# Kernel optimization log

Hardware: AMD Instinct MI355X
Metric: run time of the kernel (lower is better)

Reference implementation:

```python
import jax, jax.numpy as jnp
import numpy as np
import math

M = 0.5
S = 64.0
COS_M = math.cos(M)
SIN_M = math.sin(M)
THRESHOLD = math.cos(math.pi - M)
MM = math.sin(math.pi - M) * M

B, D, N_CLASSES = 512, 512, 100000


def setup_inputs() -> dict:
    key = jax.random.key(0)
    k1, k2, k3 = jax.random.split(key, 3)
    embeddings = jax.random.normal(k1, (B, D), dtype=jnp.float32)
    labels = jax.random.randint(k2, (B,), 0, N_CLASSES, dtype=jnp.int32)
    kernel = jax.random.normal(k3, (D, N_CLASSES), dtype=jnp.float32) * 0.05
    t = jnp.zeros((), dtype=jnp.float32)
    return {"embeddings": embeddings, "labels": labels, "kernel": kernel, "t": t}


def reference(embeddings, labels, kernel, t):
    # L2 normalize embeddings (rows) and kernel (columns)
    emb = embeddings / jnp.linalg.norm(embeddings, axis=1, keepdims=True)
    kn = kernel / jnp.linalg.norm(kernel, axis=0, keepdims=True)
    cos_theta = jnp.clip(emb @ kn, -1.0, 1.0)  # [B, C]

    b = cos_theta.shape[0]
    rows = jnp.arange(b)
    target_logit = cos_theta[rows, labels][:, None]  # [B, 1]
    sin_theta = jnp.sqrt(1.0 - jnp.square(target_logit))
    cos_theta_m = target_logit * COS_M - sin_theta * SIN_M  # [B, 1]

    mask = cos_theta > cos_theta_m  # [B, C] hard examples
    final_target_logit = jnp.where(target_logit > THRESHOLD,
                                   cos_theta_m, target_logit - MM)  # [B, 1]

    # EMA update of t (assigned before the hard-example scaling in TF code)
    new_t = 0.01 * jnp.mean(target_logit) + 0.99 * t

    # hard examples: c -> c * (t + c); others unchanged
    cos_theta = jnp.where(mask, cos_theta * (new_t + cos_theta), cos_theta)
    # overwrite label column with the margin-adjusted target logit
    cos_theta = cos_theta.at[rows, labels].set(final_target_logit[:, 0])
    return cos_theta * S
```

## Files before the change

### kernel.cpp

```cpp
#include <hip/hip_runtime.h>
#include <hip/hip_bf16.h>
#include <cstdint>
#include <cstddef>

#define C_N 100000
#define B_N 512
#define D_N 512

#define COS_M_F   0.87758256189037276f
#define SIN_M_F   0.47942553860420301f
#define THRESH_F  (-0.87758256189037276f)
#define MM_F      0.23971276930210150f
#define S_F       64.0f

typedef __attribute__((ext_vector_type(8))) short short8;
typedef __attribute__((ext_vector_type(4))) float f32x4;

__device__ __forceinline__ unsigned short f2bf(float f) {
  unsigned u = __float_as_uint(f);
  u = u + 0x7fffu + ((u >> 16) & 1u);
  return (unsigned short)(u >> 16);
}

__device__ __forceinline__ float wave_sum(float v) {
#pragma unroll
  for (int o = 32; o > 0; o >>= 1) v += __shfl_down(v, o, 64);
  return v;
}

__device__ __forceinline__ void lds_load16(const void* g, void* l) {
  __builtin_amdgcn_global_load_lds(
      (const __attribute__((address_space(1))) unsigned int*)g,
      (__attribute__((address_space(3))) unsigned int*)l, 16, 0, 0);
}

__launch_bounds__(512)
__global__ void knorm2_k(const float* __restrict__ Kp, float* __restrict__ cninv,
                         unsigned short* __restrict__ Knt) {
  __shared__ __align__(16) unsigned short Tl[64 * 512];
  __shared__ float ssum[32][64];
  __shared__ float cns[64];

  const int t = threadIdx.x;
  const int j0 = blockIdx.x * 64;
  const int jq = t & 15;
  const int dr = t >> 4;
  const int jcol = min((j0 >> 2) + jq, (C_N >> 2) - 1);
  const float4* __restrict__ Kv = (const float4*)Kp;

  float4 v[16];
#pragma unroll
  for (int i = 0; i < 16; ++i)
    v[i] = Kv[(size_t)(dr * 16 + i) * (C_N / 4) + jcol];

  float s0 = 0.f, s1 = 0.f, s2 = 0.f, s3 = 0.f;
#pragma unroll
  for (int i = 0; i < 16; ++i) {
    s0 = fmaf(v[i].x, v[i].x, s0);
    s1 = fmaf(v[i].y, v[i].y, s1);
    s2 = fmaf(v[i].z, v[i].z, s2);
    s3 = fmaf(v[i].w, v[i].w, s3);
  }
  ssum[dr][jq * 4 + 0] = s0;
  ssum[dr][jq * 4 + 1] = s1;
  ssum[dr][jq * 4 + 2] = s2;
  ssum[dr][jq * 4 + 3] = s3;
  __syncthreads();
  if (t < 64) {
    float s = 0.f;
#pragma unroll
    for (int d = 0; d < 32; ++d) s += ssum[d][t];
    float r = rsqrtf(fmaxf(s, 1e-30f));
    cns[t] = r;
    if (j0 + t < C_N) cninv[j0 + t] = r;
  }
  __syncthreads();

  const float r0 = cns[jq * 4 + 0];
  const float r1 = cns[jq * 4 + 1];
  const float r2 = cns[jq * 4 + 2];
  const float r3 = cns[jq * 4 + 3];
#pragma unroll
  for (int g = 0; g < 4; ++g) {
    const int ch = dr * 2 + (g >> 1);
    const int sub = (g & 1) * 8;
#pragma unroll
    for (int c = 0; c < 4; ++c) {
      const int j = jq * 4 + c;
      const float rc = (c == 0) ? r0 : (c == 1) ? r1 : (c == 2) ? r2 : r3;
      unsigned lo, hi;
      lo = (unsigned)f2bf(v[g * 4 + 0][c] * rc) | ((unsigned)f2bf(v[g * 4 + 1][c] * rc) << 16);
      hi = (unsigned)f2bf(v[g * 4 + 2][c] * rc) | ((unsigned)f2bf(v[g * 4 + 3][c] * rc) << 16);
      const int phys = ch ^ (j & 7);
      *(uint2*)((char*)Tl + j * 1024 + phys * 16 + sub) = make_uint2(lo, hi);
    }
  }
  __syncthreads();

  const int jr = t >> 3;
  const int dc = t & 7;
  const int jg = j0 + jr;
  if (jg < C_N) {
#pragma unroll
    for (int s = 0; s < 8; ++s) {
      const int phys = (s * 8) + (dc ^ (jr & 7));
      uint4 val = *(const uint4*)((const char*)Tl + jr * 1024 + phys * 16);
      *(uint4*)(&Knt[(size_t)jg * D_N + s * 64 + dc * 8]) = val;
    }
  }
}

__global__ void embnorm_k(const float* __restrict__ emb, unsigned short* __restrict__ embn,
                          float* __restrict__ rinv) {
  int row = blockIdx.x;
  int t = threadIdx.x;
  float4 v = ((const float4*)(emb + (size_t)row * D_N))[t];
  float ss = v.x * v.x + v.y * v.y + v.z * v.z + v.w * v.w;
  ss = wave_sum(ss);
  __shared__ float red[2];
  if ((t & 63) == 0) red[t >> 6] = ss;
  __syncthreads();
  float tot = red[0] + red[1];
  float ri = rsqrtf(tot);
  if (t == 0) rinv[row] = ri;
  ushort4 o;
  o.x = f2bf(v.x * ri); o.y = f2bf(v.y * ri); o.z = f2bf(v.z * ri); o.w = f2bf(v.w * ri);
  ((ushort4*)(embn + (size_t)row * D_N))[t] = o;
}

__global__ void target2_k(const float* __restrict__ emb, const float* __restrict__ Kp,
                          const float* __restrict__ rinv, const int* __restrict__ labels,
                          float* __restrict__ target, float* __restrict__ ctm,
                          float* __restrict__ ft) {
  int row = blockIdx.x;
  int t = threadIdx.x;
  int lab = labels[row];
  float p = 0.f, ss = 0.f;
  for (int d = t; d < D_N; d += 256) {
    float kv = Kp[(size_t)d * C_N + lab];
    p = fmaf(emb[(size_t)row * D_N + d], kv, p);
    ss = fmaf(kv, kv, ss);
  }
  p = wave_sum(p);
  ss = wave_sum(ss);
  __shared__ float redp[4], reds[4];
  if ((t & 63) == 0) { redp[t >> 6] = p; reds[t >> 6] = ss; }
  __syncthreads();
  if (t == 0) {
    float dot = redp[0] + redp[1] + redp[2] + redp[3];
    float sums = reds[0] + reds[1] + reds[2] + reds[3];
    float tg = dot * rinv[row] * rsqrtf(fmaxf(sums, 1e-30f));
    tg = fminf(fmaxf(tg, -1.f), 1.f);
    float st = sqrtf(fmaxf(1.f - tg * tg, 0.f));
    float cm = tg * COS_M_F - st * SIN_M_F;
    float f = (tg > THRESH_F) ? cm : (tg - MM_F);
    target[row] = tg;
    ctm[row] = cm;
    ft[row] = f;
  }
}

__global__ void newt_k(const float* __restrict__ target, const float* __restrict__ t_in,
                       float* __restrict__ newt) {
  int t = threadIdx.x;
  float v = target[t];
  v = wave_sum(v);
  __shared__ float red[8];
  if ((t & 63) == 0) red[t >> 6] = v;
  __syncthreads();
  if (t == 0) {
    float s = 0.f;
#pragma unroll
    for (int i = 0; i < 8; ++i) s += red[i];
    *newt = 0.01f * (s / (float)B_N) + 0.99f * t_in[0];
  }
}

__launch_bounds__(256, 4)
__global__ void gemm10_k(const unsigned short* __restrict__ Knt,
                         const unsigned short* __restrict__ embn,
                         const int* __restrict__ labels,
                         const float* __restrict__ ctm, const float* __restrict__ ft,
                         const float* __restrict__ newt_p, float* __restrict__ out) {
  __shared__ __align__(16) unsigned short Al[2][8192];
  __shared__ __align__(16) unsigned short Bb[2][2048];

  const int t = threadIdx.x;
  const int l = t & 63, w = t >> 6;
  const int mi = blockIdx.x & 1;
  const int jb = blockIdx.x >> 1;
  const int m0 = mi * 256;
  const int j0 = jb * 64;

  const int sidx = (l & 7) ^ (l >> 3);
  const int r0 = ((l >> 3) << 1) | (sidx >> 2);
  const int kc8 = (sidx & 3) * 8;

  const unsigned short* asrc = embn + (size_t)(m0 + w * 64 + r0) * D_N + kc8;
  const unsigned short* bsrc = Knt + (size_t)(j0 + w * 16 + r0) * D_N + kc8;

#pragma unroll
  for (int p = 0; p < 4; ++p)
    lds_load16(asrc + p * 16 * D_N, &Al[0][w * 2048 + p * 512]);
  lds_load16(bsrc, &Bb[0][w * 512]);
  __syncthreads();

  const int wr = w >> 1, wc = w & 1;
  const int lq = l >> 4, lr = l & 15;
  const int s16 = ((((lr & 1) << 2) | lq) ^ (lr >> 1)) << 4;
  const int rh = lr >> 1;

  f32x4 acc[8][2];
#pragma unroll
  for (int mb = 0; mb < 8; ++mb) {
    acc[mb][0] = 0;
    acc[mb][1] = 0;
  }

#pragma unroll
  for (int it = 0; it < 16; ++it) {
    const int cur = it & 1, nxt = cur ^ 1;
    if (it < 15) {
      const int k0 = (it + 1) * 32;
#pragma unroll
      for (int p = 0; p < 4; ++p)
        lds_load16(asrc + p * 16 * D_N + k0, &Al[nxt][w * 2048 + p * 512]);
      lds_load16(bsrc + k0, &Bb[nxt][w * 512]);
    }
    const char* Ab = (const char*)Al[cur];
    const char* Bt = (const char*)Bb[cur];
    short8 b0 = *(const short8*)(Bt + ((wc * 16 + 0 + rh) << 7) + s16);
    short8 b1 = *(const short8*)(Bt + ((wc * 16 + 8 + rh) << 7) + s16);
#pragma unroll
    for (int mb = 0; mb < 8; ++mb) {
      short8 a = *(const short8*)(Ab + ((wr * 64 + mb * 8 + rh) << 7) + s16);
      acc[mb][0] = __builtin_amdgcn_mfma_f32_16x16x32_bf16(a, b0, acc[mb][0], 0, 0, 0);
      acc[mb][1] = __builtin_amdgcn_mfma_f32_16x16x32_bf16(a, b1, acc[mb][1], 0, 0, 0);
    }
    __syncthreads();
  }

  const float newt = *newt_p;
  const int jn0 = j0 + wc * 32 + lr;
  const int jn1 = jn0 + 16;
#pragma unroll
  for (int mb = 0; mb < 8; ++mb) {
    const int ibase = wr * 128 + mb * 16 + 4 * lq;
#pragma unroll
    for (int r = 0; r < 4; ++r) {
      const int grow = m0 + ibase + r;
      const int lab = labels[grow];
      const float cm = ctm[grow];
      const float f = ft[grow];
      {
        float c = fminf(fmaxf(acc[mb][0][r], -1.f), 1.f);
        float o = (c > cm) ? c * (newt + c) : c;
        o = (jn0 == lab) ? f : o;
        if (jn0 < C_N) out[(size_t)grow * C_N + jn0] = o * S_F;
      }
      {
        float c = fminf(fmaxf(acc[mb][1][r], -1.f), 1.f);
        float o = (c > cm) ? c * (newt + c) : c;
        o = (jn1 == lab) ? f : o;
        if (jn1 < C_N) out[(size_t)grow * C_N + jn1] = o * S_F;
      }
    }
  }
}

extern "C" void kernel_launch(void* const* d_in, const int* in_sizes, int n_in,
                              void* d_out, int out_size, void* d_ws, size_t ws_size,
                              hipStream_t stream) {
  (void)in_sizes; (void)n_in; (void)out_size; (void)ws_size;
  const float* emb = (const float*)d_in[0];
  const int* labels = (const int*)d_in[1];
  const float* Kp = (const float*)d_in[2];
  const float* t_in = (const float*)d_in[3];
  float* out = (float*)d_out;

  char* wsp = (char*)d_ws;
  const size_t KNT_BYTES = (size_t)100096 * D_N * 2;
  unsigned short* Knt = (unsigned short*)(wsp + 0);
  unsigned short* embn = (unsigned short*)(wsp + KNT_BYTES);
  float* cninv  = (float*)(wsp + KNT_BYTES + 524288);
  float* target = (float*)(wsp + KNT_BYTES + 524288 + 400000);
  float* ctm    = (float*)(wsp + KNT_BYTES + 524288 + 400000 + 2048);
  float* ft     = (float*)(wsp + KNT_BYTES + 524288 + 400000 + 2 * 2048);
  float* rinv   = (float*)(wsp + KNT_BYTES + 524288 + 400000 + 3 * 2048);
  float* newt   = (float*)(wsp + KNT_BYTES + 524288 + 400000 + 4 * 2048);

  knorm2_k<<<(C_N + 63) / 64, 512, 0, stream>>>(Kp, cninv, Knt);
  embnorm_k<<<B_N, 128, 0, stream>>>(emb, embn, rinv);
  target2_k<<<B_N, 256, 0, stream>>>(emb, Kp, rinv, labels, target, ctm, ft);
  newt_k<<<1, 512, 0, stream>>>(target, t_in, newt);
  const int jblocks = (C_N + 63) / 64;
  gemm10_k<<<jblocks * 2, 256, 0, stream>>>(Knt, embn, labels, ctm, ft, newt, out);
}
```

Measured before the change: 194.2 us.

## Deepen GEMM load pipeline to triple-buffered A and quad-buffered B stages

Replaces the double-buffered LDS pipeline in the fused GEMM/epilogue kernel with a 3-stage A buffer and 4-stage B buffer. Loads are issued two or three iterations ahead, and synchronisation is managed by hand with explicit vmcnt waits and raw barriers instead of __syncthreads. The goal is to hide global-to-LDS latency better. In exchange it uses more LDS, and the launch bound drops from 4 to 2 blocks per CU, which may reduce occupancy. The hand-counted waits are fragile.

```diff
diff --git a/kernel.cpp b/kernel.cpp
--- a/kernel.cpp
+++ b/kernel.cpp
@@ -176,14 +176,14 @@
   }
 }
 
-__launch_bounds__(256, 4)
-__global__ void gemm10_k(const unsigned short* __restrict__ Knt,
+__launch_bounds__(256, 2)
+__global__ void gemm11_k(const unsigned short* __restrict__ Knt,
                          const unsigned short* __restrict__ embn,
                          const int* __restrict__ labels,
                          const float* __restrict__ ctm, const float* __restrict__ ft,
                          const float* __restrict__ newt_p, float* __restrict__ out) {
-  __shared__ __align__(16) unsigned short Al[2][8192];
-  __shared__ __align__(16) unsigned short Bb[2][2048];
+  __shared__ __align__(16) unsigned short Al[3][8192];
+  __shared__ __align__(16) unsigned short Bq[4][2048];
 
   const int t = threadIdx.x;
   const int l = t & 63, w = t >> 6;
@@ -199,11 +199,22 @@
   const unsigned short* asrc = embn + (size_t)(m0 + w * 64 + r0) * D_N + kc8;
   const unsigned short* bsrc = Knt + (size_t)(j0 + w * 16 + r0) * D_N + kc8;
 
-#pragma unroll
-  for (int p = 0; p < 4; ++p)
-    lds_load16(asrc + p * 16 * D_N, &Al[0][w * 2048 + p * 512]);
-  lds_load16(bsrc, &Bb[0][w * 512]);
-  __syncthreads();
+#define STAGE_A11(it)                                                          \
+  do {                                                                         \
+    const int k0_ = (it) * 32;                                                 \
+    unsigned short* d_ = &Al[(it) % 3][w * 2048];                              \
+    lds_load16(asrc + k0_, d_);                                                \
+    lds_load16(asrc + 16 * D_N + k0_, d_ + 512);                               \
+    lds_load16(asrc + 32 * D_N + k0_, d_ + 1024);                              \
+    lds_load16(asrc + 48 * D_N + k0_, d_ + 1536);                              \
+  } while (0)
+#define STAGE_B11(it) lds_load16(bsrc + (it) * 32, &Bq[(it) & 3][w * 512])
+
+  STAGE_A11(0);
+  STAGE_B11(0);
+  STAGE_B11(1);
+  STAGE_B11(2);
+  STAGE_A11(1);
 
   const int wr = w >> 1, wc = w & 1;
   const int lq = l >> 4, lr = l & 15;
@@ -219,16 +230,22 @@
 
 #pragma unroll
   for (int it = 0; it < 16; ++it) {
-    const int cur = it & 1, nxt = cur ^ 1;
-    if (it < 15) {
-      const int k0 = (it + 1) * 32;
-#pragma unroll
-      for (int p = 0; p < 4; ++p)
-        lds_load16(asrc + p * 16 * D_N + k0, &Al[nxt][w * 2048 + p * 512]);
-      lds_load16(bsrc + k0, &Bb[nxt][w * 512]);
-    }
-    const char* Ab = (const char*)Al[cur];
-    const char* Bt = (const char*)Bb[cur];
+    if (it == 15) {
+      asm volatile("s_waitcnt vmcnt(0)" ::: "memory");
+    } else if (it == 1 || it == 14) {
+      asm volatile("s_waitcnt vmcnt(5)" ::: "memory");
+    } else {
+      asm volatile("s_waitcnt vmcnt(6)" ::: "memory");
+    }
+    __builtin_amdgcn_sched_barrier(0);
+    __builtin_amdgcn_s_barrier();
+    __builtin_amdgcn_sched_barrier(0);
+
+    if (it <= 13) STAGE_A11(it + 2);
+    if (it <= 12) STAGE_B11(it + 3);
+
+    const char* Ab = (const char*)Al[it % 3];
+    const char* Bt = (const char*)Bq[it & 3];
     short8 b0 = *(const short8*)(Bt + ((wc * 16 + 0 + rh) << 7) + s16);
     short8 b1 = *(const short8*)(Bt + ((wc * 16 + 8 + rh) << 7) + s16);
 #pragma unroll
@@ -237,8 +254,13 @@
       acc[mb][0] = __builtin_amdgcn_mfma_f32_16x16x32_bf16(a, b0, acc[mb][0], 0, 0, 0);
       acc[mb][1] = __builtin_amdgcn_mfma_f32_16x16x32_bf16(a, b1, acc[mb][1], 0, 0, 0);
     }
-    __syncthreads();
-  }
+    asm volatile("s_waitcnt lgkmcnt(0)" ::: "memory");
+    __builtin_amdgcn_sched_barrier(0);
+    __builtin_amdgcn_s_barrier();
+    __builtin_amdgcn_sched_barrier(0);
+  }
+#undef STAGE_A11
+#undef STAGE_B11
 
   const float newt = *newt_p;
   const int jn0 = j0 + wc * 32 + lr;
@@ -294,5 +316,5 @@
   target2_k<<<B_N, 256, 0, stream>>>(emb, Kp, rinv, labels, target, ctm, ft);
   newt_k<<<1, 512, 0, stream>>>(target, t_in, newt);
   const int jblocks = (C_N + 63) / 64;
-  gemm10_k<<<jblocks * 2, 256, 0, stream>>>(Knt, embn, labels, ctm, ft, newt, out);
-}
+  gemm11_k<<<jblocks * 2, 256, 0, stream>>>(Knt, embn, labels, ctm, ft, newt, out);
+}
```

Result: slower. 213.3 us (+9.8%).

## Restructure GEMM tiles: full-K embedding tile in LDS, B streamed from registers, XCD-aware block order

Applied to the files above, without the earlier changes.

The GEMM kernel now uses 512-thread blocks, each covering 64 embedding rows by 256 classes instead of 256 rows by 64 classes. The whole 64x512 embedding tile is loaded into LDS once. Kernel columns are read straight from global memory into registers with a four-deep prefetch, which removes the per-iteration LDS double-buffer and its barrier. Block indices are remapped so that consecutive work groups on the same XCD share kernel tiles, improving L2 reuse of the large K matrix. The risk is higher register pressure and global latency that the prefetch does not fully hide, since B loads now skip LDS.

```diff
diff --git a/kernel.cpp b/kernel.cpp
--- a/kernel.cpp
+++ b/kernel.cpp
@@ -176,93 +176,95 @@
   }
 }
 
-__launch_bounds__(256, 4)
-__global__ void gemm10_k(const unsigned short* __restrict__ Knt,
+__launch_bounds__(512, 4)
+__global__ void gemm12_k(const unsigned short* __restrict__ Knt,
                          const unsigned short* __restrict__ embn,
                          const int* __restrict__ labels,
                          const float* __restrict__ ctm, const float* __restrict__ ft,
                          const float* __restrict__ newt_p, float* __restrict__ out) {
-  __shared__ __align__(16) unsigned short Al[2][8192];
-  __shared__ __align__(16) unsigned short Bb[2][2048];
+  __shared__ __align__(16) unsigned short A[32768];
 
   const int t = threadIdx.x;
   const int l = t & 63, w = t >> 6;
-  const int mi = blockIdx.x & 1;
-  const int jb = blockIdx.x >> 1;
-  const int m0 = mi * 256;
-  const int j0 = jb * 64;
+
+  const int nwg = gridDim.x;
+  const int q = nwg >> 3, r = nwg & 7;
+  const int xcd = blockIdx.x & 7, seq = blockIdx.x >> 3;
+  const int wg = (xcd < r ? xcd * (q + 1) : r * (q + 1) + (xcd - r) * q) + seq;
+  const int mi = wg & 7, jt = wg >> 3;
+  const int m0 = mi * 64;
+  const int j0 = jt * 256;
 
   const int sidx = (l & 7) ^ (l >> 3);
   const int r0 = ((l >> 3) << 1) | (sidx >> 2);
   const int kc8 = (sidx & 3) * 8;
-
-  const unsigned short* asrc = embn + (size_t)(m0 + w * 64 + r0) * D_N + kc8;
-  const unsigned short* bsrc = Knt + (size_t)(j0 + w * 16 + r0) * D_N + kc8;
-
-#pragma unroll
-  for (int p = 0; p < 4; ++p)
-    lds_load16(asrc + p * 16 * D_N, &Al[0][w * 2048 + p * 512]);
-  lds_load16(bsrc, &Bb[0][w * 512]);
-  __syncthreads();
-
-  const int wr = w >> 1, wc = w & 1;
+  {
+    const int c0 = w * 2;
+#pragma unroll
+    for (int cc = 0; cc < 2; ++cc) {
+      const int c = c0 + cc;
+#pragma unroll
+      for (int g = 0; g < 4; ++g)
+        lds_load16(embn + (size_t)(m0 + g * 16 + r0) * D_N + c * 32 + kc8,
+                   (char*)A + c * 4096 + g * 1024 + l * 16);
+    }
+  }
+  __syncthreads();
+
   const int lq = l >> 4, lr = l & 15;
   const int s16 = ((((lr & 1) << 2) | lq) ^ (lr >> 1)) << 4;
   const int rh = lr >> 1;
 
-  f32x4 acc[8][2];
-#pragma unroll
-  for (int mb = 0; mb < 8; ++mb) {
+  const unsigned short* b0p = Knt + (size_t)(j0 + w * 32 + lr) * D_N + lq * 8;
+  const unsigned short* b1p = b0p + (size_t)16 * D_N;
+
+  f32x4 acc[4][2];
+#pragma unroll
+  for (int mb = 0; mb < 4; ++mb) {
     acc[mb][0] = 0;
     acc[mb][1] = 0;
   }
 
+  short8 pb0[4], pb1[4];
+#pragma unroll
+  for (int p = 0; p < 4; ++p) {
+    pb0[p] = *(const short8*)(b0p + p * 32);
+    pb1[p] = *(const short8*)(b1p + p * 32);
+  }
+
 #pragma unroll
   for (int it = 0; it < 16; ++it) {
-    const int cur = it & 1, nxt = cur ^ 1;
-    if (it < 15) {
-      const int k0 = (it + 1) * 32;
-#pragma unroll
-      for (int p = 0; p < 4; ++p)
-        lds_load16(asrc + p * 16 * D_N + k0, &Al[nxt][w * 2048 + p * 512]);
-      lds_load16(bsrc + k0, &Bb[nxt][w * 512]);
-    }
-    const char* Ab = (const char*)Al[cur];
-    const char* Bt = (const char*)Bb[cur];
-    short8 b0 = *(const short8*)(Bt + ((wc * 16 + 0 + rh) << 7) + s16);
-    short8 b1 = *(const short8*)(Bt + ((wc * 16 + 8 + rh) << 7) + s16);
-#pragma unroll
-    for (int mb = 0; mb < 8; ++mb) {
-      short8 a = *(const short8*)(Ab + ((wr * 64 + mb * 8 + rh) << 7) + s16);
+    short8 b0 = pb0[it & 3];
+    short8 b1 = pb1[it & 3];
+    if (it < 12) {
+      pb0[it & 3] = *(const short8*)(b0p + (it + 4) * 32);
+      pb1[it & 3] = *(const short8*)(b1p + (it + 4) * 32);
+    }
+    const char* Ab = (const char*)A + it * 4096;
+#pragma unroll
+    for (int mb = 0; mb < 4; ++mb) {
+      short8 a = *(const short8*)(Ab + ((mb * 8 + rh) << 7) + s16);
       acc[mb][0] = __builtin_amdgcn_mfma_f32_16x16x32_bf16(a, b0, acc[mb][0], 0, 0, 0);
       acc[mb][1] = __builtin_amdgcn_mfma_f32_16x16x32_bf16(a, b1, acc[mb][1], 0, 0, 0);
     }
-    __syncthreads();
   }
 
   const float newt = *newt_p;
-  const int jn0 = j0 + wc * 32 + lr;
-  const int jn1 = jn0 + 16;
-#pragma unroll
-  for (int mb = 0; mb < 8; ++mb) {
-    const int ibase = wr * 128 + mb * 16 + 4 * lq;
-#pragma unroll
-    for (int r = 0; r < 4; ++r) {
-      const int grow = m0 + ibase + r;
+#pragma unroll
+  for (int mb = 0; mb < 4; ++mb) {
+#pragma unroll
+    for (int rr = 0; rr < 4; ++rr) {
+      const int grow = m0 + mb * 16 + lq * 4 + rr;
       const int lab = labels[grow];
       const float cm = ctm[grow];
       const float f = ft[grow];
-      {
-        float c = fminf(fmaxf(acc[mb][0][r], -1.f), 1.f);
+#pragma unroll
+      for (int nb = 0; nb < 2; ++nb) {
+        const int jn = j0 + w * 32 + nb * 16 + lr;
+        float c = fminf(fmaxf(acc[mb][nb][rr], -1.f), 1.f);
         float o = (c > cm) ? c * (newt + c) : c;
-        o = (jn0 == lab) ? f : o;
-        if (jn0 < C_N) out[(size_t)grow * C_N + jn0] = o * S_F;
-      }
-      {
-        float c = fminf(fmaxf(acc[mb][1][r], -1.f), 1.f);
-        float o = (c > cm) ? c * (newt + c) : c;
-        o = (jn1 == lab) ? f : o;
-        if (jn1 < C_N) out[(size_t)grow * C_N + jn1] = o * S_F;
+        o = (jn == lab) ? f : o;
+        if (jn < C_N) out[(size_t)grow * C_N + jn] = o * S_F;
       }
     }
   }
@@ -293,6 +295,6 @@
   embnorm_k<<<B_N, 128, 0, stream>>>(emb, embn, rinv);
   target2_k<<<B_N, 256, 0, stream>>>(emb, Kp, rinv, labels, target, ctm, ft);
   newt_k<<<1, 512, 0, stream>>>(target, t_in, newt);
-  const int jblocks = (C_N + 63) / 64;
-  gemm10_k<<<jblocks * 2, 256, 0, stream>>>(Knt, embn, labels, ctm, ft, newt, out);
-}
+  const int jt = (C_N + 255) / 256;
+  gemm12_k<<<jt * 8, 512, 0, stream>>>(Knt, embn, labels, ctm, ft, newt, out);
+}
```

Measured after the change: 233.2 us. 20.1% more time.
